# Kernel optimization log

Measured on AMD Instinct MI355X. Metric: run time of the kernel, lower is better.

## Reference

```python
import jax, jax.numpy as jnp
import numpy as np

NEG_BIG = -9e15

def setup_inputs() -> dict:
    key = jax.random.key(0)
    k1, k2, k3, k4 = jax.random.split(key, 4)
    N, F_in, F_out = 8192, 512, 128
    return {
        "input": jax.random.normal(k1, (N, F_in), dtype=jnp.float32),
        "adj": jax.random.randint(k2, (N, N), 0, 2, dtype=jnp.int32),
        "W": jax.random.normal(k3, (F_in, F_out), dtype=jnp.float32) * 0.05,
        "a": jax.random.normal(k4, (2 * F_out, 1), dtype=jnp.float32) * 0.05,
    }

def reference(input, adj, W, a):
    alpha = 0.2  # LeakyReLU negative slope
    h = input @ W                      # [N, F_out]
    F_out = h.shape[1]
    # concat score decomposition: a^T [h_i || h_j] = h_i @ a1 + h_j @ a2
    a1 = a[:F_out, 0]                  # [F_out]
    a2 = a[F_out:, 0]                  # [F_out]
    e = jax.nn.leaky_relu(h @ a1[:, None] + (h @ a2)[None, :], negative_slope=alpha)  # [N, N]
    e = jnp.where(adj > 0, e, NEG_BIG)
    attention = jax.nn.softmax(e, axis=1)
    h_prime = attention @ h            # [N, F_out]
    return jax.nn.elu(h_prime)         # concat=True
```

## Files before the change

### kernel.cpp

```cpp
#include <hip/hip_runtime.h>
#include <hip/hip_bf16.h>


typedef __attribute__((ext_vector_type(4))) float f32x4;
typedef __attribute__((ext_vector_type(8))) short s16x8;

#define N_NODES 8192
#define F_IN 512
#define F_OUT 128
#define JS 8

static __device__ __forceinline__ short f2bf(float f) {
  __hip_bfloat16 h = __float2bfloat16(f);
  return __builtin_bit_cast(short, h);
}

__global__ __launch_bounds__(256) void kMask(const int* __restrict__ adj,
    unsigned long long* __restrict__ mask) {
  const int nwaves = gridDim.x * 4;
  int wid = blockIdx.x * 4 + (threadIdx.x >> 6);
  int lane = threadIdx.x & 63;
  const int ntasks = N_NODES * (N_NODES / 256);
  for (int task = wid; task < ntasks; task += nwaves) {
    int row = task >> 5;
    int cg = task & 31;
    const int* p = adj + (size_t)row * N_NODES + cg * 256 + lane;
    int v0 = p[0], v1 = p[64], v2 = p[128], v3 = p[192];
    unsigned long long b0 = __ballot(v0 != 0);
    unsigned long long b1 = __ballot(v1 != 0);
    unsigned long long b2 = __ballot(v2 != 0);
    unsigned long long b3 = __ballot(v3 != 0);
    if (lane == 0) {
      unsigned long long* q = mask + (size_t)row * (N_NODES / 64) + cg * 4;
      ulonglong2 w0; w0.x = b0; w0.y = b1;
      ulonglong2 w1; w1.x = b2; w1.y = b3;
      *(ulonglong2*)(q) = w0;
      *(ulonglong2*)(q + 2) = w1;
    }
  }
}

__global__ __launch_bounds__(256) void kA(const float* __restrict__ W,
    const float* __restrict__ a, unsigned short* __restrict__ WT,
    float* __restrict__ wa) {
  int b = blockIdx.x;
  if (b < 256) {
    int idx = b * 256 + threadIdx.x;
    int k = idx >> 7, f = idx & 127;
    WT[(size_t)f * F_IN + k] = (unsigned short)f2bf(W[idx]);
  } else {
    int k = (b - 256) * 256 + threadIdx.x;
    if (k < F_IN) {
      const float* Wr = W + (size_t)k * F_OUT;
      float d1 = 0.f, d2 = 0.f;
#pragma unroll 8
      for (int f = 0; f < F_OUT; f += 4) {
        f32x4 w  = *(const f32x4*)(Wr + f);
        f32x4 a1 = *(const f32x4*)(a + f);
        f32x4 a2 = *(const f32x4*)(a + F_OUT + f);
        d1 += w[0] * a1[0] + w[1] * a1[1] + w[2] * a1[2] + w[3] * a1[3];
        d2 += w[0] * a2[0] + w[1] * a2[1] + w[2] * a2[2] + w[3] * a2[3];
      }
      wa[k] = d1;
      wa[F_IN + k] = d2;
    }
  }
}

__global__ __launch_bounds__(256) void kStage(const float* __restrict__ X,
    const float* __restrict__ wa, const unsigned short* __restrict__ WT,
    f32x4* __restrict__ rowdat, unsigned* __restrict__ pE,
    unsigned short* __restrict__ blob) {
  int b = blockIdx.x;
  int wave = threadIdx.x >> 6, lane = threadIdx.x & 63;

  if (b < 1024) {
    int lrow = lane & 15, grp = lane >> 4;
    int tile = b * 4 + wave;
    int fb = tile & 7;
    int nb = tile >> 3;
    const unsigned short* Ar = WT + (size_t)(fb * 16 + lrow) * F_IN + grp * 8;
    const float* Br = X + (size_t)(nb * 16 + lrow) * F_IN + grp * 8;

    f32x4 acc = (f32x4)(0.0f);
#pragma unroll
    for (int k0 = 0; k0 < F_IN; k0 += 32) {
      s16x8 af = *(const s16x8*)(Ar + k0);
      f32x4 b0 = *(const f32x4*)(Br + k0);
      f32x4 b1 = *(const f32x4*)(Br + k0 + 4);
      s16x8 bf;
#pragma unroll
      for (int e = 0; e < 4; e++) { bf[e] = f2bf(b0[e]); bf[e + 4] = f2bf(b1[e]); }
      acc = __builtin_amdgcn_mfma_f32_16x16x32_bf16(af, bf, acc, 0, 0, 0);
    }
    int cc = (nb & 1) * 16 + lrow;
    size_t bl = ((size_t)(fb * 256 + (nb >> 1)) * 64 + (cc >> 3) * 16 + grp * 4);
#pragma unroll
    for (int r = 0; r < 4; r++)
      blob[(bl + r) * 8 + (lrow & 7)] = (unsigned short)f2bf(acc[r]);
  } else {
    int i = (b - 1024) * 4 + wave;
    const float* Xr = X + (size_t)i * F_IN + lane * 8;
    f32x4 x0 = ((const f32x4*)Xr)[0];
    f32x4 x1 = ((const f32x4*)Xr)[1];
    f32x4 w10 = ((const f32x4*)(wa + lane * 8))[0];
    f32x4 w11 = ((const f32x4*)(wa + lane * 8))[1];
    f32x4 w20 = ((const f32x4*)(wa + F_IN + lane * 8))[0];
    f32x4 w21 = ((const f32x4*)(wa + F_IN + lane * 8))[1];
    float d1 = 0.f, d2 = 0.f;
#pragma unroll
    for (int e = 0; e < 4; e++) {
      d1 += x0[e] * w10[e] + x1[e] * w11[e];
      d2 += x0[e] * w20[e] + x1[e] * w21[e];
    }
#pragma unroll
    for (int m = 1; m < 64; m <<= 1) {
      d1 += __shfl_xor(d1, m, 64);
      d2 += __shfl_xor(d2, m, 64);
    }
    if (lane == 0) {
      float s1 = d1, s2 = d2;
      f32x4 rd;
      rd[0] = expf(s1);
      rd[1] = expf(0.2f * s1);
      rd[2] = expf(-s1);
      rd[3] = 0.f;
      rowdat[i] = rd;
      unsigned e2  = (unsigned)(unsigned short)f2bf(expf(s2));
      unsigned e2s = (unsigned)(unsigned short)f2bf(expf(0.2f * s2));
      pE[i] = (e2s << 16) | e2;
    }
  }
}

__global__ __launch_bounds__(256, 4) void kCompute(
    const unsigned* __restrict__ mask32, const unsigned short* __restrict__ blob,
    const f32x4* __restrict__ rowdat, const unsigned* __restrict__ pE,
    float* __restrict__ accws, float* __restrict__ denws) {
  int wave = threadIdx.x >> 6, lane = threadIdx.x & 63;
  int lrow = lane & 15, grp = lane >> 4;
  int rb = blockIdx.x >> 3;
  int js = blockIdx.x & 7;
  int row = rb * 64 + wave * 16 + lrow;

  f32x4 rd = rowdat[row];
  float E1 = rd[0], E1s = rd[1], T1 = rd[2];

  f32x4 acc[8];
#pragma unroll
  for (int nt = 0; nt < 8; nt++) acc[nt] = (f32x4)(0.0f);
  float dsum = 0.f;

  const unsigned* mrow = mask32 + (size_t)row * (N_NODES / 32) + js * 32;

  for (int o = 0; o < 4; o++) {
    uint4 cm0 = *(const uint4*)(mrow + o * 8);
    uint4 cm1 = *(const uint4*)(mrow + o * 8 + 4);

#pragma unroll
    for (int c = 0; c < 8; c++) {
      int ct = js * 32 + o * 8 + c;
      int j0 = ct * 32 + grp * 8;
      unsigned w = (c < 4) ? cm0[c] : cm1[c - 4];
      unsigned b8 = (w >> (grp * 8)) & 0xffu;
      uint4 P0 = *(const uint4*)(pE + j0);
      uint4 P1 = *(const uint4*)(pE + j0 + 4);
      s16x8 af;
#define PROCE(pw, e)                                                  \
      {                                                               \
        unsigned pu = (pw);                                           \
        float E2  = __builtin_bit_cast(float, pu << 16);              \
        float E2s = __builtin_bit_cast(float, pu & 0xffff0000u);      \
        float sel = (E2 > T1) ? E1 * E2 : E1s * E2s;                  \
        float p = ((b8 >> (e)) & 1u) ? sel : 0.f;                     \
        dsum += p;                                                    \
        af[e] = f2bf(p);                                              \
      }
      PROCE(P0.x, 0) PROCE(P0.y, 1) PROCE(P0.z, 2) PROCE(P0.w, 3)
      PROCE(P1.x, 4) PROCE(P1.y, 5) PROCE(P1.z, 6) PROCE(P1.w, 7)
#undef PROCE
#pragma unroll
      for (int nt = 0; nt < 8; nt++) {
        s16x8 bf = *(const s16x8*)(blob +
            (((size_t)nt * 256 + ct) * 64 + lane) * 8);
        acc[nt] = __builtin_amdgcn_mfma_f32_16x16x32_bf16(af, bf, acc[nt], 0, 0, 0);
      }
    }
  }

  dsum += __shfl_xor(dsum, 16, 64);
  dsum += __shfl_xor(dsum, 32, 64);
  if (lane < 16)
    denws[js * N_NODES + rb * 64 + wave * 16 + lane] = dsum;

#pragma unroll
  for (int nt = 0; nt < 8; nt++)
#pragma unroll
    for (int r = 0; r < 4; r++)
      accws[((size_t)js * N_NODES + rb * 64 + wave * 16 + grp * 4 + r) * F_OUT +
            nt * 16 + lrow] = acc[nt][r];
}

__global__ void kD(const float* __restrict__ accws,
                   const float* __restrict__ denws, float* __restrict__ out) {
  int idx4 = blockIdx.x * 256 + threadIdx.x;
  int i = idx4 >> 5;
  const int S4 = N_NODES * F_OUT / 4;
  f32x4 s = (f32x4)(0.0f);
  float d = 0.f;
#pragma unroll
  for (int q = 0; q < JS; q++) {
    s += ((const f32x4*)accws)[idx4 + (size_t)q * S4];
    d += denws[i + q * N_NODES];
  }
  f32x4 v = s / d;
#pragma unroll
  for (int e = 0; e < 4; e++) v[e] = v[e] > 0.f ? v[e] : expm1f(v[e]);
  ((f32x4*)out)[idx4] = v;
}

extern "C" void kernel_launch(void* const* d_in, const int* in_sizes, int n_in,
                              void* d_out, int out_size, void* d_ws, size_t ws_size,
                              hipStream_t stream) {
  const float* X   = (const float*)d_in[0];
  const int*   adj = (const int*)d_in[1];
  const float* W   = (const float*)d_in[2];
  const float* a   = (const float*)d_in[3];
  float* out = (float*)d_out;

  char* ws = (char*)d_ws;
  size_t off = 0;
  unsigned short* WT = (unsigned short*)(ws + off); off += (size_t)F_OUT * F_IN * 2;
  unsigned short* blob = (unsigned short*)(ws + off); off += (size_t)F_OUT * N_NODES * 2;
  f32x4* rowdat = (f32x4*)(ws + off); off += (size_t)N_NODES * 16;
  unsigned* pE = (unsigned*)(ws + off); off += (size_t)N_NODES * 4;
  float* wa = (float*)(ws + off); off += (size_t)2 * F_IN * 4;
  unsigned long long* mask = (unsigned long long*)(ws + off);
  off += (size_t)N_NODES * (N_NODES / 64) * 8;
  float* accws = (float*)(ws + off); off += (size_t)JS * N_NODES * F_OUT * 4;
  float* denws = (float*)(ws + off); off += (size_t)JS * N_NODES * 4;
  (void)in_sizes; (void)n_in; (void)out_size; (void)ws_size;

  kMask<<<2048, 256, 0, stream>>>(adj, mask);
  kA<<<258, 256, 0, stream>>>(W, a, WT, wa);
  kStage<<<3072, 256, 0, stream>>>(X, wa, WT, rowdat, pE, blob);
  kCompute<<<(N_NODES / 64) * JS, 256, 0, stream>>>((const unsigned*)mask, blob,
                                                    rowdat, pE, accws, denws);
  kD<<<(N_NODES * F_OUT) / 4 / 256, 256, 0, stream>>>(accws, denws, out);
}
```

Measured before the change: 486.4 us.

## Fuse mask build into staging kernel and split compute work across feature halves

Merges the adjacency-bitmask kernel into the staging kernel so mask building and the h/score staging share one launch and can overlap. kCompute now gives each block 32 rows, with waves split across two 64-wide feature groups, which halves the per-wave accumulator count and doubles the grid. The main loop is software-pipelined: pE and blob fragments for the next column tile are loaded before the MFMA step of the current tile. The cost is that each pair of waves repeats the same probability/mask computation, and mask bits plus pE are read twice as often.

```diff
diff --git a/kernel.cpp b/kernel.cpp
--- a/kernel.cpp
+++ b/kernel.cpp
@@ -13,31 +13,6 @@
 static __device__ __forceinline__ short f2bf(float f) {
   __hip_bfloat16 h = __float2bfloat16(f);
   return __builtin_bit_cast(short, h);
-}
-
-__global__ __launch_bounds__(256) void kMask(const int* __restrict__ adj,
-    unsigned long long* __restrict__ mask) {
-  const int nwaves = gridDim.x * 4;
-  int wid = blockIdx.x * 4 + (threadIdx.x >> 6);
-  int lane = threadIdx.x & 63;
-  const int ntasks = N_NODES * (N_NODES / 256);
-  for (int task = wid; task < ntasks; task += nwaves) {
-    int row = task >> 5;
-    int cg = task & 31;
-    const int* p = adj + (size_t)row * N_NODES + cg * 256 + lane;
-    int v0 = p[0], v1 = p[64], v2 = p[128], v3 = p[192];
-    unsigned long long b0 = __ballot(v0 != 0);
-    unsigned long long b1 = __ballot(v1 != 0);
-    unsigned long long b2 = __ballot(v2 != 0);
-    unsigned long long b3 = __ballot(v3 != 0);
-    if (lane == 0) {
-      unsigned long long* q = mask + (size_t)row * (N_NODES / 64) + cg * 4;
-      ulonglong2 w0; w0.x = b0; w0.y = b1;
-      ulonglong2 w1; w1.x = b2; w1.y = b3;
-      *(ulonglong2*)(q) = w0;
-      *(ulonglong2*)(q + 2) = w1;
-    }
-  }
 }
 
 __global__ __launch_bounds__(256) void kA(const float* __restrict__ W,
@@ -67,16 +42,38 @@
   }
 }
 
-__global__ __launch_bounds__(256) void kStage(const float* __restrict__ X,
+__global__ __launch_bounds__(256) void kPrep(const int* __restrict__ adj,
+    unsigned long long* __restrict__ mask, const float* __restrict__ X,
     const float* __restrict__ wa, const unsigned short* __restrict__ WT,
     f32x4* __restrict__ rowdat, unsigned* __restrict__ pE,
     unsigned short* __restrict__ blob) {
   int b = blockIdx.x;
   int wave = threadIdx.x >> 6, lane = threadIdx.x & 63;
 
-  if (b < 1024) {
+  if (b < 4096) {
+    const int nwaves = 4096 * 4;
+    int wid = b * 4 + wave;
+    const int ntasks = N_NODES * (N_NODES / 256);
+    for (int task = wid; task < ntasks; task += nwaves) {
+      int row = task >> 5;
+      int cg = task & 31;
+      const int* p = adj + (size_t)row * N_NODES + cg * 256 + lane;
+      int v0 = p[0], v1 = p[64], v2 = p[128], v3 = p[192];
+      unsigned long long b0 = __ballot(v0 != 0);
+      unsigned long long b1 = __ballot(v1 != 0);
+      unsigned long long b2 = __ballot(v2 != 0);
+      unsigned long long b3 = __ballot(v3 != 0);
+      if (lane == 0) {
+        unsigned long long* q = mask + (size_t)row * (N_NODES / 64) + cg * 4;
+        ulonglong2 w0; w0.x = b0; w0.y = b1;
+        ulonglong2 w1; w1.x = b2; w1.y = b3;
+        *(ulonglong2*)(q) = w0;
+        *(ulonglong2*)(q + 2) = w1;
+      }
+    }
+  } else if (b < 5120) {
     int lrow = lane & 15, grp = lane >> 4;
-    int tile = b * 4 + wave;
+    int tile = (b - 4096) * 4 + wave;
     int fb = tile & 7;
     int nb = tile >> 3;
     const unsigned short* Ar = WT + (size_t)(fb * 16 + lrow) * F_IN + grp * 8;
@@ -99,7 +96,7 @@
     for (int r = 0; r < 4; r++)
       blob[(bl + r) * 8 + (lrow & 7)] = (unsigned short)f2bf(acc[r]);
   } else {
-    int i = (b - 1024) * 4 + wave;
+    int i = (b - 5120) * 4 + wave;
     const float* Xr = X + (size_t)i * F_IN + lane * 8;
     f32x4 x0 = ((const f32x4*)Xr)[0];
     f32x4 x1 = ((const f32x4*)Xr)[1];
@@ -141,31 +138,33 @@
   int lrow = lane & 15, grp = lane >> 4;
   int rb = blockIdx.x >> 3;
   int js = blockIdx.x & 7;
-  int row = rb * 64 + wave * 16 + lrow;
+  int rt01 = wave & 1, fg = wave >> 1;
+  int row = rb * 32 + rt01 * 16 + lrow;
 
   f32x4 rd = rowdat[row];
   float E1 = rd[0], E1s = rd[1], T1 = rd[2];
 
-  f32x4 acc[8];
-#pragma unroll
-  for (int nt = 0; nt < 8; nt++) acc[nt] = (f32x4)(0.0f);
+  f32x4 acc[4];
+#pragma unroll
+  for (int nt = 0; nt < 4; nt++) acc[nt] = (f32x4)(0.0f);
   float dsum = 0.f;
 
   const unsigned* mrow = mask32 + (size_t)row * (N_NODES / 32) + js * 32;
-
-  for (int o = 0; o < 4; o++) {
-    uint4 cm0 = *(const uint4*)(mrow + o * 8);
-    uint4 cm1 = *(const uint4*)(mrow + o * 8 + 4);
-
-#pragma unroll
-    for (int c = 0; c < 8; c++) {
-      int ct = js * 32 + o * 8 + c;
-      int j0 = ct * 32 + grp * 8;
-      unsigned w = (c < 4) ? cm0[c] : cm1[c - 4];
-      unsigned b8 = (w >> (grp * 8)) & 0xffu;
-      uint4 P0 = *(const uint4*)(pE + j0);
-      uint4 P1 = *(const uint4*)(pE + j0 + 4);
-      s16x8 af;
+  const unsigned* pEw = pE + js * 1024 + grp * 8;
+  const unsigned short* blobW =
+      blob + (((size_t)fg * 4 * 256 + js * 32) * 64 + lane) * 8;
+
+  uint4 P0a, P1a, P0b, P1b;
+  s16x8 Ba0, Ba1, Ba2, Ba3, Bb0, Bb1, Bb2, Bb3;
+
+#define LOADP(P0, P1, c)                                              \
+  { P0 = *(const uint4*)(pEw + (c) * 32);                             \
+    P1 = *(const uint4*)(pEw + (c) * 32 + 4); }
+#define LOADB(B0, B1, B2, B3, c)                                      \
+  { B0 = *(const s16x8*)(blobW + ((size_t)0 * 256 + (c)) * 512);      \
+    B1 = *(const s16x8*)(blobW + ((size_t)1 * 256 + (c)) * 512);      \
+    B2 = *(const s16x8*)(blobW + ((size_t)2 * 256 + (c)) * 512);      \
+    B3 = *(const s16x8*)(blobW + ((size_t)3 * 256 + (c)) * 512); }
 #define PROCE(pw, e)                                                  \
       {                                                               \
         unsigned pu = (pw);                                           \
@@ -176,29 +175,53 @@
         dsum += p;                                                    \
         af[e] = f2bf(p);                                              \
       }
-      PROCE(P0.x, 0) PROCE(P0.y, 1) PROCE(P0.z, 2) PROCE(P0.w, 3)
-      PROCE(P1.x, 4) PROCE(P1.y, 5) PROCE(P1.z, 6) PROCE(P1.w, 7)
+#define STEP(PA, PB, B0, B1, B2, B3, MW)                              \
+  {                                                                   \
+    unsigned b8 = ((MW) >> (grp * 8)) & 0xffu;                        \
+    s16x8 af;                                                         \
+    PROCE(PA.x, 0) PROCE(PA.y, 1) PROCE(PA.z, 2) PROCE(PA.w, 3)       \
+    PROCE(PB.x, 4) PROCE(PB.y, 5) PROCE(PB.z, 6) PROCE(PB.w, 7)       \
+    acc[0] = __builtin_amdgcn_mfma_f32_16x16x32_bf16(af, B0, acc[0], 0, 0, 0); \
+    acc[1] = __builtin_amdgcn_mfma_f32_16x16x32_bf16(af, B1, acc[1], 0, 0, 0); \
+    acc[2] = __builtin_amdgcn_mfma_f32_16x16x32_bf16(af, B2, acc[2], 0, 0, 0); \
+    acc[3] = __builtin_amdgcn_mfma_f32_16x16x32_bf16(af, B3, acc[3], 0, 0, 0); \
+  }
+
+  LOADP(P0a, P1a, 0)
+  LOADB(Ba0, Ba1, Ba2, Ba3, 0)
+
+  for (int o = 0; o < 4; o++) {
+    uint4 cm0 = *(const uint4*)(mrow + o * 8);
+    uint4 cm1 = *(const uint4*)(mrow + o * 8 + 4);
+#pragma unroll
+    for (int cc = 0; cc < 8; cc += 2) {
+      int c = o * 8 + cc;
+      unsigned mEven = (cc < 4) ? cm0[cc] : cm1[cc - 4];
+      unsigned mOdd  = (cc + 1 < 4) ? cm0[cc + 1] : cm1[cc - 3];
+      LOADP(P0b, P1b, (c + 1) & 31)
+      LOADB(Bb0, Bb1, Bb2, Bb3, (c + 1) & 31)
+      STEP(P0a, P1a, Ba0, Ba1, Ba2, Ba3, mEven)
+      LOADP(P0a, P1a, (c + 2) & 31)
+      LOADB(Ba0, Ba1, Ba2, Ba3, (c + 2) & 31)
+      STEP(P0b, P1b, Bb0, Bb1, Bb2, Bb3, mOdd)
+    }
+  }
+#undef STEP
 #undef PROCE
-#pragma unroll
-      for (int nt = 0; nt < 8; nt++) {
-        s16x8 bf = *(const s16x8*)(blob +
-            (((size_t)nt * 256 + ct) * 64 + lane) * 8);
-        acc[nt] = __builtin_amdgcn_mfma_f32_16x16x32_bf16(af, bf, acc[nt], 0, 0, 0);
-      }
-    }
-  }
+#undef LOADB
+#undef LOADP
 
   dsum += __shfl_xor(dsum, 16, 64);
   dsum += __shfl_xor(dsum, 32, 64);
-  if (lane < 16)
-    denws[js * N_NODES + rb * 64 + wave * 16 + lane] = dsum;
-
-#pragma unroll
-  for (int nt = 0; nt < 8; nt++)
+  if (fg == 0 && lane < 16)
+    denws[js * N_NODES + rb * 32 + rt01 * 16 + lane] = dsum;
+
+#pragma unroll
+  for (int nt = 0; nt < 4; nt++)
 #pragma unroll
     for (int r = 0; r < 4; r++)
-      accws[((size_t)js * N_NODES + rb * 64 + wave * 16 + grp * 4 + r) * F_OUT +
-            nt * 16 + lrow] = acc[nt][r];
+      accws[((size_t)js * N_NODES + rb * 32 + rt01 * 16 + grp * 4 + r) * F_OUT +
+            fg * 64 + nt * 16 + lrow] = acc[nt][r];
 }
 
 __global__ void kD(const float* __restrict__ accws,
@@ -241,10 +264,9 @@
   float* denws = (float*)(ws + off); off += (size_t)JS * N_NODES * 4;
   (void)in_sizes; (void)n_in; (void)out_size; (void)ws_size;
 
-  kMask<<<2048, 256, 0, stream>>>(adj, mask);
   kA<<<258, 256, 0, stream>>>(W, a, WT, wa);
-  kStage<<<3072, 256, 0, stream>>>(X, wa, WT, rowdat, pE, blob);
-  kCompute<<<(N_NODES / 64) * JS, 256, 0, stream>>>((const unsigned*)mask, blob,
+  kPrep<<<7168, 256, 0, stream>>>(adj, mask, X, wa, WT, rowdat, pE, blob);
+  kCompute<<<(N_NODES / 32) * JS, 256, 0, stream>>>((const unsigned*)mask, blob,
                                                     rowdat, pE, accws, denws);
   kD<<<(N_NODES * F_OUT) / 4 / 256, 256, 0, stream>>>(accws, denws, out);
 }
```

Result: no change. 478.9 us (-1.5%).

## Stage h tiles through double-buffered LDS and fuse mask build into prep kernel

Applied to the files above, without the earlier changes.

The compute kernel now stages each group of h (bf16) tiles into a 64KB double-buffered LDS region using global_load_lds, prefetching the next group while MFMAs run on the current one. To make these copies contiguous, the blob layout is reordered by column-split, group and feature tile. The adjacency mask build is merged into the staging kernel as an extra block range, which removes one launch and lets it run alongside the projection GEMM. In exchange, LDS use cuts occupancy and each group adds a block-wide barrier.

```diff
diff --git a/kernel.cpp b/kernel.cpp
--- a/kernel.cpp
+++ b/kernel.cpp
@@ -15,29 +15,10 @@
   return __builtin_bit_cast(short, h);
 }
 
-__global__ __launch_bounds__(256) void kMask(const int* __restrict__ adj,
-    unsigned long long* __restrict__ mask) {
-  const int nwaves = gridDim.x * 4;
-  int wid = blockIdx.x * 4 + (threadIdx.x >> 6);
-  int lane = threadIdx.x & 63;
-  const int ntasks = N_NODES * (N_NODES / 256);
-  for (int task = wid; task < ntasks; task += nwaves) {
-    int row = task >> 5;
-    int cg = task & 31;
-    const int* p = adj + (size_t)row * N_NODES + cg * 256 + lane;
-    int v0 = p[0], v1 = p[64], v2 = p[128], v3 = p[192];
-    unsigned long long b0 = __ballot(v0 != 0);
-    unsigned long long b1 = __ballot(v1 != 0);
-    unsigned long long b2 = __ballot(v2 != 0);
-    unsigned long long b3 = __ballot(v3 != 0);
-    if (lane == 0) {
-      unsigned long long* q = mask + (size_t)row * (N_NODES / 64) + cg * 4;
-      ulonglong2 w0; w0.x = b0; w0.y = b1;
-      ulonglong2 w1; w1.x = b2; w1.y = b3;
-      *(ulonglong2*)(q) = w0;
-      *(ulonglong2*)(q + 2) = w1;
-    }
-  }
+static __device__ __forceinline__ void glds16(const void* g, void* l) {
+  __builtin_amdgcn_global_load_lds(
+      (const __attribute__((address_space(1))) unsigned*)g,
+      (__attribute__((address_space(3))) unsigned*)l, 16, 0, 0);
 }
 
 __global__ __launch_bounds__(256) void kA(const float* __restrict__ W,
@@ -67,10 +48,11 @@
   }
 }
 
-__global__ __launch_bounds__(256) void kStage(const float* __restrict__ X,
+__global__ __launch_bounds__(256) void kPrep(const int* __restrict__ adj,
+    unsigned long long* __restrict__ mask, const float* __restrict__ X,
     const float* __restrict__ wa, const unsigned short* __restrict__ WT,
     f32x4* __restrict__ rowdat, unsigned* __restrict__ pE,
-    unsigned short* __restrict__ blob) {
+    unsigned short* __restrict__ blob2) {
   int b = blockIdx.x;
   int wave = threadIdx.x >> 6, lane = threadIdx.x & 63;
 
@@ -93,12 +75,20 @@
       for (int e = 0; e < 4; e++) { bf[e] = f2bf(b0[e]); bf[e + 4] = f2bf(b1[e]); }
       acc = __builtin_amdgcn_mfma_f32_16x16x32_bf16(af, bf, acc, 0, 0, 0);
     }
-    int cc = (nb & 1) * 16 + lrow;
-    size_t bl = ((size_t)(fb * 256 + (nb >> 1)) * 64 + (cc >> 3) * 16 + grp * 4);
-#pragma unroll
-    for (int r = 0; r < 4; r++)
-      blob[(bl + r) * 8 + (lrow & 7)] = (unsigned short)f2bf(acc[r]);
-  } else {
+    int c = nb * 16 + lrow;
+    int jsx = c >> 10;
+    int ctj = (c >> 5) & 31;
+    int g = ctj >> 2, ci = ctj & 3;
+    int cpos = c & 31;
+    int e = cpos & 7;
+    int lbase = (cpos >> 3) << 4;
+    size_t tbase = ((((size_t)jsx * 8 + g) * 4 + ci) * 8 + fb) * 64;
+#pragma unroll
+    for (int r = 0; r < 4; r++) {
+      int l = lbase + grp * 4 + r;
+      blob2[(tbase + l) * 8 + e] = (unsigned short)f2bf(acc[r]);
+    }
+  } else if (b < 3072) {
     int i = (b - 1024) * 4 + wave;
     const float* Xr = X + (size_t)i * F_IN + lane * 8;
     f32x4 x0 = ((const f32x4*)Xr)[0];
@@ -130,14 +120,37 @@
       unsigned e2s = (unsigned)(unsigned short)f2bf(expf(0.2f * s2));
       pE[i] = (e2s << 16) | e2;
     }
+  } else {
+    const int nwaves = 4096 * 4;
+    int wid = (b - 3072) * 4 + wave;
+    const int ntasks = N_NODES * (N_NODES / 256);
+    for (int task = wid; task < ntasks; task += nwaves) {
+      int row = task >> 5;
+      int cg = task & 31;
+      const int* p = adj + (size_t)row * N_NODES + cg * 256 + lane;
+      int v0 = p[0], v1 = p[64], v2 = p[128], v3 = p[192];
+      unsigned long long b0 = __ballot(v0 != 0);
+      unsigned long long b1 = __ballot(v1 != 0);
+      unsigned long long b2 = __ballot(v2 != 0);
+      unsigned long long b3 = __ballot(v3 != 0);
+      if (lane == 0) {
+        unsigned long long* q = mask + (size_t)row * (N_NODES / 64) + cg * 4;
+        ulonglong2 w0; w0.x = b0; w0.y = b1;
+        ulonglong2 w1; w1.x = b2; w1.y = b3;
+        *(ulonglong2*)(q) = w0;
+        *(ulonglong2*)(q + 2) = w1;
+      }
+    }
   }
 }
 
 __global__ __launch_bounds__(256, 4) void kCompute(
-    const unsigned* __restrict__ mask32, const unsigned short* __restrict__ blob,
+    const unsigned* __restrict__ mask32, const unsigned short* __restrict__ blob2,
     const f32x4* __restrict__ rowdat, const unsigned* __restrict__ pE,
     float* __restrict__ accws, float* __restrict__ denws) {
-  int wave = threadIdx.x >> 6, lane = threadIdx.x & 63;
+  __shared__ char lds[2][32768];
+  int tid = threadIdx.x;
+  int wave = tid >> 6, lane = tid & 63;
   int lrow = lane & 15, grp = lane >> 4;
   int rb = blockIdx.x >> 3;
   int js = blockIdx.x & 7;
@@ -152,19 +165,29 @@
   float dsum = 0.f;
 
   const unsigned* mrow = mask32 + (size_t)row * (N_NODES / 32) + js * 32;
-
-  for (int o = 0; o < 4; o++) {
-    uint4 cm0 = *(const uint4*)(mrow + o * 8);
-    uint4 cm1 = *(const uint4*)(mrow + o * 8 + 4);
-
-#pragma unroll
-    for (int c = 0; c < 8; c++) {
-      int ct = js * 32 + o * 8 + c;
-      int j0 = ct * 32 + grp * 8;
-      unsigned w = (c < 4) ? cm0[c] : cm1[c - 4];
-      unsigned b8 = (w >> (grp * 8)) & 0xffu;
+  const char* gbase = (const char*)blob2 + (size_t)js * 8 * 32768;
+
+#pragma unroll
+  for (int r = 0; r < 8; r++)
+    glds16(gbase + r * 4096 + tid * 16, &lds[0][r * 4096 + tid * 16]);
+  __syncthreads();
+
+  int cur = 0;
+  for (int g = 0; g < 8; g++) {
+    if (g < 7) {
+      const char* gsrc = gbase + (size_t)(g + 1) * 32768;
+      char* ldst = &lds[cur ^ 1][0];
+#pragma unroll
+      for (int r = 0; r < 8; r++)
+        glds16(gsrc + r * 4096 + tid * 16, ldst + r * 4096 + tid * 16);
+    }
+    uint4 mm = *(const uint4*)(mrow + g * 4);
+#pragma unroll
+    for (int ci = 0; ci < 4; ci++) {
+      int j0 = (js * 32 + g * 4 + ci) * 32 + grp * 8;
       uint4 P0 = *(const uint4*)(pE + j0);
       uint4 P1 = *(const uint4*)(pE + j0 + 4);
+      unsigned b8 = (mm[ci] >> (grp * 8)) & 0xffu;
       s16x8 af;
 #define PROCE(pw, e)                                                  \
       {                                                               \
@@ -181,11 +204,12 @@
 #undef PROCE
 #pragma unroll
       for (int nt = 0; nt < 8; nt++) {
-        s16x8 bf = *(const s16x8*)(blob +
-            (((size_t)nt * 256 + ct) * 64 + lane) * 8);
+        s16x8 bf = *(const s16x8*)(&lds[cur][(ci * 8 + nt) * 1024 + lane * 16]);
         acc[nt] = __builtin_amdgcn_mfma_f32_16x16x32_bf16(af, bf, acc[nt], 0, 0, 0);
       }
     }
+    __syncthreads();
+    cur ^= 1;
   }
 
   dsum += __shfl_xor(dsum, 16, 64);
@@ -231,7 +255,7 @@
   char* ws = (char*)d_ws;
   size_t off = 0;
   unsigned short* WT = (unsigned short*)(ws + off); off += (size_t)F_OUT * F_IN * 2;
-  unsigned short* blob = (unsigned short*)(ws + off); off += (size_t)F_OUT * N_NODES * 2;
+  unsigned short* blob2 = (unsigned short*)(ws + off); off += (size_t)F_OUT * N_NODES * 2;
   f32x4* rowdat = (f32x4*)(ws + off); off += (size_t)N_NODES * 16;
   unsigned* pE = (unsigned*)(ws + off); off += (size_t)N_NODES * 4;
   float* wa = (float*)(ws + off); off += (size_t)2 * F_IN * 4;
@@ -241,10 +265,9 @@
   float* denws = (float*)(ws + off); off += (size_t)JS * N_NODES * 4;
   (void)in_sizes; (void)n_in; (void)out_size; (void)ws_size;
 
-  kMask<<<2048, 256, 0, stream>>>(adj, mask);
   kA<<<258, 256, 0, stream>>>(W, a, WT, wa);
-  kStage<<<3072, 256, 0, stream>>>(X, wa, WT, rowdat, pE, blob);
-  kCompute<<<(N_NODES / 64) * JS, 256, 0, stream>>>((const unsigned*)mask, blob,
+  kPrep<<<7168, 256, 0, stream>>>(adj, mask, X, wa, WT, rowdat, pE, blob2);
+  kCompute<<<(N_NODES / 64) * JS, 256, 0, stream>>>((const unsigned*)mask, blob2,
                                                     rowdat, pE, accws, denws);
   kD<<<(N_NODES * F_OUT) / 4 / 256, 256, 0, stream>>>(accws, denws, out);
 }
```

Result: faster. 457.3 us (-6.0%).
